# Kernel optimization log

Measured on AMD Instinct MI355X. Metric: run time of the kernel, lower is better.

## Reference

```python
import jax, jax.numpy as jnp
import numpy as np

B, S, D_MODEL, D_K, D_V, H = 2, 2048, 1024, 1024, 1024, 16


def setup_inputs() -> dict:
    key = jax.random.key(0)
    ks = jax.random.split(key, 12)
    s = 0.02
    inp = {
        "queries": jax.random.normal(ks[0], (B, S, D_MODEL), jnp.float32),
        "keys": jax.random.normal(ks[1], (B, S, D_MODEL), jnp.float32),
        "values": jax.random.normal(ks[2], (B, S, D_MODEL), jnp.float32),
        # causal mask: 1 where attention is disallowed (added as -1e9*mask)
        "mask": jnp.triu(jnp.ones((1, 1, S, S), jnp.float32), k=1),
        "Wq": jax.random.normal(ks[3], (D_MODEL, D_K), jnp.float32) * s,
        "bq": jnp.zeros((D_K,), jnp.float32),
        "Wk": jax.random.normal(ks[4], (D_MODEL, D_K), jnp.float32) * s,
        "bk": jnp.zeros((D_K,), jnp.float32),
        "Wv": jax.random.normal(ks[5], (D_MODEL, D_V), jnp.float32) * s,
        "bv": jnp.zeros((D_V,), jnp.float32),
        "Wo": jax.random.normal(ks[6], (D_K, D_MODEL), jnp.float32) * s,
        "bo": jnp.zeros((D_MODEL,), jnp.float32),
    }
    return inp


def _split_heads(x):  # [B,S,D] -> [B,H,S,D/H]
    b, s, d = x.shape
    return x.reshape(b, s, H, d // H).transpose(0, 2, 1, 3)


def reference(queries, keys, values, mask, Wq, bq, Wk, bk, Wv, bv, Wo, bo):
    q = _split_heads(queries @ Wq + bq)   # [B,H,S,hd]
    k = _split_heads(keys @ Wk + bk)
    v = _split_heads(values @ Wv + bv)
    # NOTE: original scales by sqrt(full d_k), not per-head dim (faithful quirk)
    scores = jnp.einsum("bhqd,bhkd->bhqk", q, k) / jnp.sqrt(jnp.float32(D_K))
    scores = scores + (-1e9) * mask
    w = jax.nn.softmax(scores, axis=-1)
    out = jnp.einsum("bhqk,bhkd->bhqd", w, v)        # [B,H,S,hd]
    out = out.transpose(0, 2, 1, 3).reshape(q.shape[0], q.shape[2], D_K)
    return out @ Wo + bo
```

## Files before the change

### kernel.cpp

```cpp
#include <hip/hip_runtime.h>
#include <hip/hip_bf16.h>
#include <cstdint>

typedef __bf16 bf16;
typedef __bf16 bf16x2 __attribute__((ext_vector_type(2)));
typedef __bf16 bf16x4 __attribute__((ext_vector_type(4)));
typedef __bf16 bf16x8 __attribute__((ext_vector_type(8)));
typedef float f32x4 __attribute__((ext_vector_type(4)));

#define B_ 2
#define S_ 2048
#define DM 1024
#define H_ 16
#define HD 64

__device__ __forceinline__ void gload_lds16(const bf16* g, bf16* l) {
  __builtin_amdgcn_global_load_lds((const __attribute__((address_space(1))) void*)g,
                                   (__attribute__((address_space(3))) void*)l,
                                   16, 0, 0);
}

__global__ __launch_bounds__(256) void convert_k(const float* __restrict__ s0,
                                                 const float* __restrict__ s1,
                                                 const float* __restrict__ s2,
                                                 bf16* __restrict__ d0,
                                                 bf16* __restrict__ d1,
                                                 bf16* __restrict__ d2) {
  const float* s = (blockIdx.z == 0) ? s0 : (blockIdx.z == 1) ? s1 : s2;
  bf16* d = (blockIdx.z == 0) ? d0 : (blockIdx.z == 1) ? d1 : d2;
  const size_t i = ((size_t)blockIdx.x * 256 + threadIdx.x) * 8;
  f32x4 a = *(const f32x4*)(s + i);
  f32x4 b = *(const f32x4*)(s + i + 4);
  bf16x8 o;
#pragma unroll
  for (int j = 0; j < 4; j++) { o[j] = (bf16)a[j]; o[j + 4] = (bf16)b[j]; }
  *(bf16x8*)(d + i) = o;
}

__global__ __launch_bounds__(256) void transposeW_k(
    const float* __restrict__ w0, const float* __restrict__ w1,
    const float* __restrict__ w2, const float* __restrict__ w3,
    bf16* __restrict__ t0, bf16* __restrict__ t1,
    bf16* __restrict__ t2, bf16* __restrict__ t3) {
  const float* src = (blockIdx.z == 0) ? w0 : (blockIdx.z == 1) ? w1
                     : (blockIdx.z == 2) ? w2 : w3;
  bf16* dst = (blockIdx.z == 0) ? t0 : (blockIdx.z == 1) ? t1
              : (blockIdx.z == 2) ? t2 : t3;
  __shared__ float tile[32][33];
  const int tx = threadIdx.x, ty = threadIdx.y;
  const int x0 = blockIdx.x * 32, y0 = blockIdx.y * 32;
#pragma unroll
  for (int r = 0; r < 4; r++)
    tile[ty + r * 8][tx] = src[(size_t)(y0 + ty + r * 8) * DM + x0 + tx];
  __syncthreads();
#pragma unroll
  for (int r = 0; r < 4; r++)
    dst[(size_t)(x0 + ty + r * 8) * DM + y0 + tx] = (bf16)tile[tx][ty + r * 8];
}

struct GArgs { const void* A; const bf16* Bt; const float* bias; void* C; };
struct GArgs3 { GArgs g[3]; };

template <bool AF32, bool CF32>
__global__ __launch_bounds__(256) void gemm_k(GArgs3 args, int M, int N, int K) {
  const GArgs ga = args.g[blockIdx.z];
  __shared__ __align__(16) bf16 As[128 * 32];
  __shared__ __align__(16) bf16 Bs[128 * 32];
  const int tid = threadIdx.x;
  const int lane = tid & 63, w = tid >> 6;
  const int l15 = lane & 15, q = lane >> 4;
  const int wr = w >> 1, wc = w & 1;
  const int m0 = blockIdx.y * 128, n0 = blockIdx.x * 128;

  const int c0 = w * 128 + lane;
  const int c1 = c0 + 64;
  const int r0 = c0 >> 2, r1 = c1 >> 2, koff = (c0 & 3) * 8;
  const bf16* gB0 = ga.Bt + (size_t)(n0 + r0) * K + koff;
  const bf16* gB1 = ga.Bt + (size_t)(n0 + r1) * K + koff;
  bf16* lA0 = As + (w * 2 + 0) * 512;
  bf16* lA1 = As + (w * 2 + 1) * 512;
  bf16* lB0 = Bs + (w * 2 + 0) * 512;
  bf16* lB1 = Bs + (w * 2 + 1) * 512;

  const float* pA0 = nullptr;
  const float* pA1 = nullptr;
  f32x4 t00, t01, t10, t11;
  if constexpr (AF32) {
    const float* A = (const float*)ga.A;
    pA0 = A + (size_t)(m0 + r0) * K + koff;
    pA1 = A + (size_t)(m0 + r1) * K + koff;
    t00 = *(const f32x4*)pA0; t01 = *(const f32x4*)(pA0 + 4);
    t10 = *(const f32x4*)pA1; t11 = *(const f32x4*)(pA1 + 4);
  }

  f32x4 acc[4][4] = {};

  for (int k0 = 0; k0 < K; k0 += 32) {
    if constexpr (AF32) {
      bf16x8 va0, va1;
#pragma unroll
      for (int j = 0; j < 4; j++) {
        va0[j] = (bf16)t00[j]; va0[j + 4] = (bf16)t01[j];
        va1[j] = (bf16)t10[j]; va1[j + 4] = (bf16)t11[j];
      }
      *(bf16x8*)(lA0 + lane * 8) = va0;
      *(bf16x8*)(lA1 + lane * 8) = va1;
    } else {
      const bf16* A = (const bf16*)ga.A;
      gload_lds16(A + (size_t)(m0 + r0) * K + koff + k0, lA0);
      gload_lds16(A + (size_t)(m0 + r1) * K + koff + k0, lA1);
    }
    gload_lds16(gB0 + k0, lB0);
    gload_lds16(gB1 + k0, lB1);
    __syncthreads();

    bf16x8 a[4], b[4];
#pragma unroll
    for (int mt = 0; mt < 4; mt++)
      a[mt] = *(const bf16x8*)(As + (wr * 64 + mt * 16 + l15) * 32 + q * 8);
#pragma unroll
    for (int nt = 0; nt < 4; nt++)
      b[nt] = *(const bf16x8*)(Bs + (wc * 64 + nt * 16 + l15) * 32 + q * 8);

    if constexpr (AF32) {
      const int kn = (k0 + 32 < K) ? k0 + 32 : k0;
      t00 = *(const f32x4*)(pA0 + kn); t01 = *(const f32x4*)(pA0 + kn + 4);
      t10 = *(const f32x4*)(pA1 + kn); t11 = *(const f32x4*)(pA1 + kn + 4);
    }

#pragma unroll
    for (int mt = 0; mt < 4; mt++)
#pragma unroll
      for (int nt = 0; nt < 4; nt++)
        acc[mt][nt] = __builtin_amdgcn_mfma_f32_16x16x32_bf16(a[mt], b[nt],
                                                              acc[mt][nt], 0, 0, 0);
    __syncthreads();
  }

#pragma unroll
  for (int nt = 0; nt < 4; nt++) {
    const int col = n0 + wc * 64 + nt * 16 + l15;
    const float bv = ga.bias[col];
#pragma unroll
    for (int mt = 0; mt < 4; mt++) {
      const int row = m0 + wr * 64 + mt * 16 + q * 4;
#pragma unroll
      for (int r = 0; r < 4; r++) {
        const float val = acc[mt][nt][r] + bv;
        if constexpr (CF32)
          ((float*)ga.C)[(size_t)(row + r) * N + col] = val;
        else
          ((bf16*)ga.C)[(size_t)(row + r) * N + col] = (bf16)val;
      }
    }
  }
}

__global__ __launch_bounds__(256) void attn_k(const bf16* Qp, const bf16* Kp,
                                              const bf16* Vp, bf16* Op) {
  const int b = blockIdx.z, h = blockIdx.y;
  const int pair = blockIdx.x;
  const int tid = threadIdx.x;
  const int lane = tid & 63, w = tid >> 6;
  const int l15 = lane & 15, q = lane >> 4;

  __shared__ __align__(16) bf16 Qs[64][72];
  __shared__ __align__(16) bf16 Ks[2][64][72];
  __shared__ __align__(16) bf16 Vts[2][64][72];
  __shared__ __align__(16) bf16 Ps[4][16][76];

  const size_t headoff = (size_t)b * S_ * DM + h * HD;
  const bf16* Kb = Kp + headoff;
  const bf16* Vb = Vp + headoff;

  const int kr0 = tid >> 3, kr1 = 32 + (tid >> 3), kcb = (tid & 7) * 8;
  const int d0 = (tid & 31) * 2, kq = (tid >> 5) * 8;
  const float QSCALE = 0.04508422f;

#pragma unroll 1
  for (int half = 0; half < 2; half++) {
    const int xt = half ? pair : 31 - pair;
    const int i0 = xt * 64;

    for (int c = tid; c < 512; c += 256) {
      const int r = c >> 3, cb = (c & 7) * 8;
      bf16x8 v = *(const bf16x8*)(Qp + headoff + (size_t)(i0 + r) * DM + cb);
      bf16x8 o;
#pragma unroll
      for (int j = 0; j < 8; j++) o[j] = (bf16)((float)v[j] * QSCALE);
      *(bf16x8*)&Qs[r][cb] = o;
    }
    {
      bf16x8 k0v = *(const bf16x8*)(Kb + (size_t)kr0 * DM + kcb);
      bf16x8 k1v = *(const bf16x8*)(Kb + (size_t)kr1 * DM + kcb);
      *(bf16x8*)&Ks[0][kr0][kcb] = k0v;
      *(bf16x8*)&Ks[0][kr1][kcb] = k1v;
      bf16x8 vlo, vhi;
#pragma unroll
      for (int j = 0; j < 8; j++) {
        bf16x2 p = *(const bf16x2*)(Vb + (size_t)(kq + j) * DM + d0);
        vlo[j] = p[0]; vhi[j] = p[1];
      }
      *(bf16x8*)&Vts[0][d0][kq] = vlo;
      *(bf16x8*)&Vts[0][d0 + 1][kq] = vhi;
    }
    __syncthreads();

    f32x4 oacc[4] = {};
    float rsum[4] = {0.f, 0.f, 0.f, 0.f};
    int buf = 0;

    for (int j0 = 0; j0 <= i0; j0 += 64, buf ^= 1) {
      const int jn = (j0 + 64 <= i0) ? j0 + 64 : 0;
      bf16x8 kpre0 = *(const bf16x8*)(Kb + (size_t)(jn + kr0) * DM + kcb);
      bf16x8 kpre1 = *(const bf16x8*)(Kb + (size_t)(jn + kr1) * DM + kcb);
      bf16x2 vpre[8];
#pragma unroll
      for (int j = 0; j < 8; j++)
        vpre[j] = *(const bf16x2*)(Vb + (size_t)(jn + kq + j) * DM + d0);

      f32x4 s[4] = {};
#pragma unroll
      for (int kk = 0; kk < 2; kk++) {
        bf16x8 a = *(const bf16x8*)&Qs[w * 16 + l15][kk * 32 + q * 8];
#pragma unroll
        for (int nt = 0; nt < 4; nt++) {
          bf16x8 bb = *(const bf16x8*)&Ks[buf][nt * 16 + l15][kk * 32 + q * 8];
          s[nt] = __builtin_amdgcn_mfma_f32_16x16x32_bf16(a, bb, s[nt], 0, 0, 0);
        }
      }

      if (j0 == i0) {
        const int row = w * 16 + q * 4;
#pragma unroll
        for (int nt = 0; nt < 4; nt++) {
          const int col = nt * 16 + l15;
#pragma unroll
          for (int r = 0; r < 4; r++) {
            float p = (col <= row + r) ? __builtin_amdgcn_exp2f(s[nt][r]) : 0.f;
            rsum[r] += p;
            s[nt][r] = p;
          }
        }
      } else {
#pragma unroll
        for (int nt = 0; nt < 4; nt++)
#pragma unroll
          for (int r = 0; r < 4; r++) {
            const float p = __builtin_amdgcn_exp2f(s[nt][r]);
            rsum[r] += p;
            s[nt][r] = p;
          }
      }

#pragma unroll
      for (int nt = 0; nt < 4; nt++)
#pragma unroll
        for (int r = 0; r < 4; r++)
          Ps[w][q * 4 + r][nt * 16 + l15] = (bf16)s[nt][r];
      asm volatile("s_waitcnt lgkmcnt(0)" ::: "memory");

#pragma unroll
      for (int kk = 0; kk < 2; kk++) {
        bf16x4 alo = *(const bf16x4*)&Ps[w][l15][kk * 32 + q * 8];
        bf16x4 ahi = *(const bf16x4*)&Ps[w][l15][kk * 32 + q * 8 + 4];
        bf16x8 a;
#pragma unroll
        for (int j = 0; j < 4; j++) { a[j] = alo[j]; a[j + 4] = ahi[j]; }
#pragma unroll
        for (int nt = 0; nt < 4; nt++) {
          bf16x8 bb = *(const bf16x8*)&Vts[buf][nt * 16 + l15][kk * 32 + q * 8];
          oacc[nt] = __builtin_amdgcn_mfma_f32_16x16x32_bf16(a, bb, oacc[nt], 0, 0, 0);
        }
      }

      *(bf16x8*)&Ks[buf ^ 1][kr0][kcb] = kpre0;
      *(bf16x8*)&Ks[buf ^ 1][kr1][kcb] = kpre1;
      {
        bf16x8 vlo, vhi;
#pragma unroll
        for (int j = 0; j < 8; j++) { vlo[j] = vpre[j][0]; vhi[j] = vpre[j][1]; }
        *(bf16x8*)&Vts[buf ^ 1][d0][kq] = vlo;
        *(bf16x8*)&Vts[buf ^ 1][d0 + 1][kq] = vhi;
      }
      __syncthreads();
    }

#pragma unroll
    for (int r = 0; r < 4; r++) {
      float t = rsum[r];
#pragma unroll
      for (int off = 1; off < 16; off <<= 1) t += __shfl_xor(t, off);
      rsum[r] = 1.0f / t;
    }
#pragma unroll
    for (int nt = 0; nt < 4; nt++) {
      const int d = nt * 16 + l15;
#pragma unroll
      for (int r = 0; r < 4; r++) {
        const int srow = i0 + w * 16 + q * 4 + r;
        Op[headoff + (size_t)srow * DM + d] = (bf16)(oacc[nt][r] * rsum[r]);
      }
    }
  }
}

extern "C" void kernel_launch(void* const* d_in, const int* in_sizes, int n_in,
                              void* d_out, int out_size, void* d_ws, size_t ws_size,
                              hipStream_t stream) {
  const float* q_in = (const float*)d_in[0];
  const float* k_in = (const float*)d_in[1];
  const float* v_in = (const float*)d_in[2];
  const float* Wq = (const float*)d_in[4];
  const float* bq = (const float*)d_in[5];
  const float* Wk = (const float*)d_in[6];
  const float* bk = (const float*)d_in[7];
  const float* Wv = (const float*)d_in[8];
  const float* bv = (const float*)d_in[9];
  const float* Wo = (const float*)d_in[10];
  const float* bo = (const float*)d_in[11];

  bf16* ws = (bf16*)d_ws;
  const size_t NQ = (size_t)B_ * S_ * DM;
  bf16* Qp = ws;
  bf16* Kp = ws + NQ;
  bf16* Vp = ws + 2 * NQ;
  bf16* WqT = ws + 3 * NQ;
  bf16* WkT = WqT + (size_t)DM * DM;
  bf16* WvT = WkT + (size_t)DM * DM;
  bf16* WoT = WvT + (size_t)DM * DM;
  bf16* qb = WoT + (size_t)DM * DM;
  bf16* kb = qb + NQ;
  bf16* vb = kb + NQ;

  const bool fast = ws_size >= (size_t)(28 * 1024 * 1024) * 2;

  transposeW_k<<<dim3(32, 32, 4), dim3(32, 8), 0, stream>>>(
      Wq, Wk, Wv, Wo, WqT, WkT, WvT, WoT);

  if (fast) {
    convert_k<<<dim3((B_ * S_ * DM) / (256 * 8), 1, 3), 256, 0, stream>>>(
        q_in, k_in, v_in, qb, kb, vb);
    GArgs3 g3;
    g3.g[0] = {qb, WqT, bq, Qp};
    g3.g[1] = {kb, WkT, bk, Kp};
    g3.g[2] = {vb, WvT, bv, Vp};
    gemm_k<false, false><<<dim3(DM / 128, (B_ * S_) / 128, 3), 256, 0, stream>>>(
        g3, B_ * S_, DM, DM);
  } else {
    GArgs3 g3;
    g3.g[0] = {q_in, WqT, bq, Qp};
    g3.g[1] = {k_in, WkT, bk, Kp};
    g3.g[2] = {v_in, WvT, bv, Vp};
    gemm_k<true, false><<<dim3(DM / 128, (B_ * S_) / 128, 3), 256, 0, stream>>>(
        g3, B_ * S_, DM, DM);
  }

  attn_k<<<dim3(16, H_, B_), 256, 0, stream>>>(Qp, Kp, Vp, Qp);

  GArgs3 gp;
  gp.g[0] = {Qp, WoT, bo, d_out};
  gp.g[1] = gp.g[0];
  gp.g[2] = gp.g[0];
  gemm_k<false, true><<<dim3(DM / 128, (B_ * S_) / 128, 1), 256, 0, stream>>>(
      gp, B_ * S_, DM, DM);
}
```

Measured before the change: 250.2 us.

## Restructure attention with 32x32 MFMA, register P exchange, and split-key waves

The attention kernel switches from 16x16x32 to 32x32x16 MFMA, with Q held in registers. The softmax probabilities are passed to the PV matmul through v_cvt_pk_bf16 and permlane32_swap instead of a round-trip through shared memory. Each wave now covers a 32-query by 32-key quadrant, so the two key-half partial outputs and row sums are reduced through shared memory at the end, and fully masked diagonal quadrants are skipped. The grid becomes 1024 blocks, one query tile each, interleaved for causal load balance instead of paired tiles, with launch bounds of 4 blocks per CU and setprio hints. The cost is an extra reduction step and more blocks, each doing uneven work.

```diff
diff --git a/kernel.cpp b/kernel.cpp
--- a/kernel.cpp
+++ b/kernel.cpp
@@ -7,6 +7,8 @@
 typedef __bf16 bf16x4 __attribute__((ext_vector_type(4)));
 typedef __bf16 bf16x8 __attribute__((ext_vector_type(8)));
 typedef float f32x4 __attribute__((ext_vector_type(4)));
+typedef float f32x16 __attribute__((ext_vector_type(16)));
+typedef unsigned int u32;
 
 #define B_ 2
 #define S_ 2048
@@ -18,6 +20,12 @@
   __builtin_amdgcn_global_load_lds((const __attribute__((address_space(1))) void*)g,
                                    (__attribute__((address_space(3))) void*)l,
                                    16, 0, 0);
+}
+
+__device__ __forceinline__ u32 cvt_pk_bf16(float lo, float hi) {
+  u32 r;
+  asm("v_cvt_pk_bf16_f32 %0, %1, %2" : "=v"(r) : "v"(lo), "v"(hi));
+  return r;
 }
 
 __global__ __launch_bounds__(256) void convert_k(const float* __restrict__ s0,
@@ -156,18 +164,27 @@
   }
 }
 
-__global__ __launch_bounds__(256) void attn_k(const bf16* Qp, const bf16* Kp,
-                                              const bf16* Vp, bf16* Op) {
-  const int b = blockIdx.z, h = blockIdx.y;
-  const int pair = blockIdx.x;
+__global__ __launch_bounds__(256, 4) void attn_k(const bf16* __restrict__ Qp,
+                                                 const bf16* __restrict__ Kp,
+                                                 const bf16* __restrict__ Vp,
+                                                 bf16* __restrict__ Op) {
+  const int g = blockIdx.x;
+  const int c = g & 255, sl = g >> 8;
+  const int u = c & 31;
+  const int xt = (sl == 0) ? u : (sl == 1) ? 31 - u
+                 : (sl == 2) ? (u ^ 16) : 31 - (u ^ 16);
+  const int h = (c >> 5) | ((sl & 1) << 3);
+  const int b = sl >> 1;
+  const int i0 = xt * 64;
+
   const int tid = threadIdx.x;
   const int lane = tid & 63, w = tid >> 6;
-  const int l15 = lane & 15, q = lane >> 4;
-
-  __shared__ __align__(16) bf16 Qs[64][72];
-  __shared__ __align__(16) bf16 Ks[2][64][72];
-  __shared__ __align__(16) bf16 Vts[2][64][72];
-  __shared__ __align__(16) bf16 Ps[4][16][76];
+  const int l31 = lane & 31, hi = lane >> 5;
+  const int qh = w >> 1, kh = w & 1;
+
+  __shared__ __align__(16) char smem[36864];
+  bf16 (*Ks)[64][72] = (bf16 (*)[64][72])smem;
+  bf16 (*Vts)[64][72] = (bf16 (*)[64][72])(smem + 18432);
 
   const size_t headoff = (size_t)b * S_ * DM + h * HD;
   const bf16* Kb = Kp + headoff;
@@ -177,130 +194,151 @@
   const int d0 = (tid & 31) * 2, kq = (tid >> 5) * 8;
   const float QSCALE = 0.04508422f;
 
-#pragma unroll 1
-  for (int half = 0; half < 2; half++) {
-    const int xt = half ? pair : 31 - pair;
-    const int i0 = xt * 64;
-
-    for (int c = tid; c < 512; c += 256) {
-      const int r = c >> 3, cb = (c & 7) * 8;
-      bf16x8 v = *(const bf16x8*)(Qp + headoff + (size_t)(i0 + r) * DM + cb);
+  bf16x8 qreg[4];
+  {
+    const bf16* qb = Qp + headoff + (size_t)(i0 + qh * 32 + l31) * DM + hi * 8;
+#pragma unroll
+    for (int kk = 0; kk < 4; kk++) {
+      bf16x8 v = *(const bf16x8*)(qb + kk * 16);
       bf16x8 o;
 #pragma unroll
       for (int j = 0; j < 8; j++) o[j] = (bf16)((float)v[j] * QSCALE);
-      *(bf16x8*)&Qs[r][cb] = o;
-    }
-    {
-      bf16x8 k0v = *(const bf16x8*)(Kb + (size_t)kr0 * DM + kcb);
-      bf16x8 k1v = *(const bf16x8*)(Kb + (size_t)kr1 * DM + kcb);
-      *(bf16x8*)&Ks[0][kr0][kcb] = k0v;
-      *(bf16x8*)&Ks[0][kr1][kcb] = k1v;
-      bf16x8 vlo, vhi;
-#pragma unroll
-      for (int j = 0; j < 8; j++) {
-        bf16x2 p = *(const bf16x2*)(Vb + (size_t)(kq + j) * DM + d0);
-        vlo[j] = p[0]; vhi[j] = p[1];
-      }
-      *(bf16x8*)&Vts[0][d0][kq] = vlo;
-      *(bf16x8*)&Vts[0][d0 + 1][kq] = vhi;
-    }
-    __syncthreads();
-
-    f32x4 oacc[4] = {};
-    float rsum[4] = {0.f, 0.f, 0.f, 0.f};
-    int buf = 0;
-
-    for (int j0 = 0; j0 <= i0; j0 += 64, buf ^= 1) {
-      const int jn = (j0 + 64 <= i0) ? j0 + 64 : 0;
-      bf16x8 kpre0 = *(const bf16x8*)(Kb + (size_t)(jn + kr0) * DM + kcb);
-      bf16x8 kpre1 = *(const bf16x8*)(Kb + (size_t)(jn + kr1) * DM + kcb);
-      bf16x2 vpre[8];
-#pragma unroll
-      for (int j = 0; j < 8; j++)
-        vpre[j] = *(const bf16x2*)(Vb + (size_t)(jn + kq + j) * DM + d0);
-
-      f32x4 s[4] = {};
-#pragma unroll
-      for (int kk = 0; kk < 2; kk++) {
-        bf16x8 a = *(const bf16x8*)&Qs[w * 16 + l15][kk * 32 + q * 8];
-#pragma unroll
-        for (int nt = 0; nt < 4; nt++) {
-          bf16x8 bb = *(const bf16x8*)&Ks[buf][nt * 16 + l15][kk * 32 + q * 8];
-          s[nt] = __builtin_amdgcn_mfma_f32_16x16x32_bf16(a, bb, s[nt], 0, 0, 0);
-        }
-      }
-
-      if (j0 == i0) {
-        const int row = w * 16 + q * 4;
-#pragma unroll
-        for (int nt = 0; nt < 4; nt++) {
-          const int col = nt * 16 + l15;
-#pragma unroll
-          for (int r = 0; r < 4; r++) {
-            float p = (col <= row + r) ? __builtin_amdgcn_exp2f(s[nt][r]) : 0.f;
-            rsum[r] += p;
-            s[nt][r] = p;
-          }
+      qreg[kk] = o;
+    }
+  }
+
+  {
+    bf16x8 k0v = *(const bf16x8*)(Kb + (size_t)kr0 * DM + kcb);
+    bf16x8 k1v = *(const bf16x8*)(Kb + (size_t)kr1 * DM + kcb);
+    *(bf16x8*)&Ks[0][kr0][kcb] = k0v;
+    *(bf16x8*)&Ks[0][kr1][kcb] = k1v;
+    bf16x8 vlo, vhi;
+#pragma unroll
+    for (int j = 0; j < 8; j++) {
+      bf16x2 p = *(const bf16x2*)(Vb + (size_t)(kq + j) * DM + d0);
+      vlo[j] = p[0]; vhi[j] = p[1];
+    }
+    *(bf16x8*)&Vts[0][d0][kq] = vlo;
+    *(bf16x8*)&Vts[0][d0 + 1][kq] = vhi;
+  }
+  __syncthreads();
+
+  f32x16 oacc0 = {}, oacc1 = {};
+  float rsum = 0.f;
+  int buf = 0;
+
+  for (int j0 = 0; j0 <= i0; j0 += 64, buf ^= 1) {
+    const int jn = (j0 + 64 <= i0) ? j0 + 64 : 0;
+    bf16x8 kpre0 = *(const bf16x8*)(Kb + (size_t)(jn + kr0) * DM + kcb);
+    bf16x8 kpre1 = *(const bf16x8*)(Kb + (size_t)(jn + kr1) * DM + kcb);
+    bf16x2 vpre[8];
+#pragma unroll
+    for (int j = 0; j < 8; j++)
+      vpre[j] = *(const bf16x2*)(Vb + (size_t)(jn + kq + j) * DM + d0);
+
+    const bool diag = (j0 == i0);
+    if (!(diag && kh > qh)) {
+      f32x16 sacc = {};
+      __builtin_amdgcn_s_setprio(1);
+#pragma unroll
+      for (int kk = 0; kk < 4; kk++) {
+        bf16x8 ka = *(const bf16x8*)&Ks[buf][kh * 32 + l31][kk * 16 + hi * 8];
+        sacc = __builtin_amdgcn_mfma_f32_32x32x16_bf16(ka, qreg[kk], sacc, 0, 0, 0);
+      }
+      __builtin_amdgcn_s_setprio(0);
+
+      float p[16];
+      if (diag) {
+        const int qrl = qh * 32 + l31;
+#pragma unroll
+        for (int r = 0; r < 16; r++) {
+          const int keyl = kh * 32 + (r & 3) + 8 * (r >> 2) + 4 * hi;
+          p[r] = (keyl <= qrl) ? __builtin_amdgcn_exp2f(sacc[r]) : 0.f;
+          rsum += p[r];
         }
       } else {
 #pragma unroll
-        for (int nt = 0; nt < 4; nt++)
-#pragma unroll
-          for (int r = 0; r < 4; r++) {
-            const float p = __builtin_amdgcn_exp2f(s[nt][r]);
-            rsum[r] += p;
-            s[nt][r] = p;
-          }
-      }
-
-#pragma unroll
-      for (int nt = 0; nt < 4; nt++)
-#pragma unroll
-        for (int r = 0; r < 4; r++)
-          Ps[w][q * 4 + r][nt * 16 + l15] = (bf16)s[nt][r];
-      asm volatile("s_waitcnt lgkmcnt(0)" ::: "memory");
-
-#pragma unroll
-      for (int kk = 0; kk < 2; kk++) {
-        bf16x4 alo = *(const bf16x4*)&Ps[w][l15][kk * 32 + q * 8];
-        bf16x4 ahi = *(const bf16x4*)&Ps[w][l15][kk * 32 + q * 8 + 4];
-        bf16x8 a;
-#pragma unroll
-        for (int j = 0; j < 4; j++) { a[j] = alo[j]; a[j + 4] = ahi[j]; }
-#pragma unroll
-        for (int nt = 0; nt < 4; nt++) {
-          bf16x8 bb = *(const bf16x8*)&Vts[buf][nt * 16 + l15][kk * 32 + q * 8];
-          oacc[nt] = __builtin_amdgcn_mfma_f32_16x16x32_bf16(a, bb, oacc[nt], 0, 0, 0);
+        for (int r = 0; r < 16; r++) {
+          p[r] = __builtin_amdgcn_exp2f(sacc[r]);
+          rsum += p[r];
         }
       }
 
-      *(bf16x8*)&Ks[buf ^ 1][kr0][kcb] = kpre0;
-      *(bf16x8*)&Ks[buf ^ 1][kr1][kcb] = kpre1;
-      {
-        bf16x8 vlo, vhi;
-#pragma unroll
-        for (int j = 0; j < 8; j++) { vlo[j] = vpre[j][0]; vhi[j] = vpre[j][1]; }
-        *(bf16x8*)&Vts[buf ^ 1][d0][kq] = vlo;
-        *(bf16x8*)&Vts[buf ^ 1][d0 + 1][kq] = vhi;
-      }
-      __syncthreads();
-    }
-
-#pragma unroll
-    for (int r = 0; r < 4; r++) {
-      float t = rsum[r];
-#pragma unroll
-      for (int off = 1; off < 16; off <<= 1) t += __shfl_xor(t, off);
-      rsum[r] = 1.0f / t;
-    }
-#pragma unroll
-    for (int nt = 0; nt < 4; nt++) {
-      const int d = nt * 16 + l15;
-#pragma unroll
-      for (int r = 0; r < 4; r++) {
-        const int srow = i0 + w * 16 + q * 4 + r;
-        Op[headoff + (size_t)srow * DM + d] = (bf16)(oacc[nt][r] * rsum[r]);
-      }
+      u32 Aq[4][2];
+#pragma unroll
+      for (int t = 0; t < 4; t++) {
+        Aq[t][0] = cvt_pk_bf16(p[4 * t + 0], p[4 * t + 1]);
+        Aq[t][1] = cvt_pk_bf16(p[4 * t + 2], p[4 * t + 3]);
+      }
+      bf16x8 pb[2];
+#pragma unroll
+      for (int s = 0; s < 2; s++) {
+        auto e0 = __builtin_amdgcn_permlane32_swap(Aq[2 * s][0], Aq[2 * s + 1][0], false, false);
+        auto e1 = __builtin_amdgcn_permlane32_swap(Aq[2 * s][1], Aq[2 * s + 1][1], false, false);
+        union { u32 u[4]; bf16x8 v; } cv;
+        cv.u[0] = e0[0]; cv.u[1] = e1[0]; cv.u[2] = e0[1]; cv.u[3] = e1[1];
+        pb[s] = cv.v;
+      }
+
+      __builtin_amdgcn_s_setprio(1);
+#pragma unroll
+      for (int s = 0; s < 2; s++) {
+        bf16x8 va0 = *(const bf16x8*)&Vts[buf][l31][kh * 32 + s * 16 + hi * 8];
+        bf16x8 va1 = *(const bf16x8*)&Vts[buf][32 + l31][kh * 32 + s * 16 + hi * 8];
+        oacc0 = __builtin_amdgcn_mfma_f32_32x32x16_bf16(va0, pb[s], oacc0, 0, 0, 0);
+        oacc1 = __builtin_amdgcn_mfma_f32_32x32x16_bf16(va1, pb[s], oacc1, 0, 0, 0);
+      }
+      __builtin_amdgcn_s_setprio(0);
+    }
+
+    *(bf16x8*)&Ks[buf ^ 1][kr0][kcb] = kpre0;
+    *(bf16x8*)&Ks[buf ^ 1][kr1][kcb] = kpre1;
+    {
+      bf16x8 vlo, vhi;
+#pragma unroll
+      for (int j = 0; j < 8; j++) { vlo[j] = vpre[j][0]; vhi[j] = vpre[j][1]; }
+      *(bf16x8*)&Vts[buf ^ 1][d0][kq] = vlo;
+      *(bf16x8*)&Vts[buf ^ 1][d0 + 1][kq] = vhi;
+    }
+    __syncthreads();
+  }
+
+  float rtot_w = rsum + __shfl_xor(rsum, 32);
+  float* osum = (float*)smem;
+  float* auxf = (float*)(smem + 32768);
+#pragma unroll
+  for (int m = 0; m < 2; m++) {
+#pragma unroll
+    for (int rq = 0; rq < 4; rq++) {
+      f32x4 v4;
+#pragma unroll
+      for (int e = 0; e < 4; e++)
+        v4[e] = m ? oacc1[rq * 4 + e] : oacc0[rq * 4 + e];
+      *(f32x4*)(osum + w * 2048 + (m * 4 + rq) * 256 + lane * 4) = v4;
+    }
+  }
+  if (lane < 32) auxf[w * 32 + lane] = rtot_w;
+  __syncthreads();
+
+  {
+    const int q = tid >> 2, q31b = q & 31, qh2 = q >> 5;
+    const float rtot = auxf[(qh2 * 2 + 0) * 32 + q31b] + auxf[(qh2 * 2 + 1) * 32 + q31b];
+    const float rinv = 1.0f / rtot;
+    const int dbase = (tid & 3) * 16;
+    bf16* orow = Op + headoff + (size_t)(i0 + q) * DM + dbase;
+#pragma unroll
+    for (int gg = 0; gg < 2; gg++) {
+      bf16x8 o8;
+#pragma unroll
+      for (int e = 0; e < 8; e++) {
+        const int d = dbase + gg * 8 + e;
+        const int base = (((d >> 5) << 2) | ((d >> 3) & 3)) * 256 +
+                         (q31b + 32 * ((d >> 2) & 1)) * 4 + (d & 3);
+        const float v = osum[(qh2 * 2 + 0) * 2048 + base] +
+                        osum[(qh2 * 2 + 1) * 2048 + base];
+        o8[e] = (bf16)(v * rinv);
+      }
+      *(bf16x8*)(orow + gg * 8) = o8;
     }
   }
 }
@@ -356,7 +394,7 @@
         g3, B_ * S_, DM, DM);
   }
 
-  attn_k<<<dim3(16, H_, B_), 256, 0, stream>>>(Qp, Kp, Vp, Qp);
+  attn_k<<<dim3(1024, 1, 1), 256, 0, stream>>>(Qp, Kp, Vp, Qp);
 
   GArgs3 gp;
   gp.g[0] = {Qp, WoT, bo, d_out};
```

After: 239.0 us. -4.5%, faster.
